# Kernel optimization log

Hardware: AMD Instinct MI355X
Metric: run time of the kernel (lower is better)

## Reference

```python
import jax, jax.numpy as jnp
import numpy as np

BN_EPS = 1e-5


def setup_inputs() -> dict:
    key = jax.random.key(0)
    ks = jax.random.split(key, 6)
    b, c_out, c_high = 8, 256, 512
    h1 = w1 = 64
    h2 = w2 = 32
    return {
        "fms_low": jax.random.normal(ks[0], (b, c_out, h1, w1), jnp.float32),
        "fms_high": jax.random.normal(ks[1], (b, c_high, h2, w2), jnp.float32),
        "w_conv": jax.random.normal(ks[2], (c_out, c_high), jnp.float32) * (1.0 / np.sqrt(c_high)),
        "bn_gamma": jnp.ones((c_out,), jnp.float32),
        "bn_beta": jnp.zeros((c_out,), jnp.float32),
        "bn_mean": jnp.zeros((c_out,), jnp.float32),
        "bn_var": jnp.ones((c_out,), jnp.float32),
        "fc1_w": jax.random.normal(ks[3], (c_out // 4, c_out), jnp.float32) * (1.0 / np.sqrt(c_out)),
        "fc1_b": jnp.zeros((c_out // 4,), jnp.float32),
        "fc2_w": jax.random.normal(ks[4], (c_out // 4, c_out), jnp.float32) * (1.0 / np.sqrt(c_out)),
        "fc2_b": jnp.zeros((c_out // 4,), jnp.float32),
        "scale": jax.random.normal(ks[5], (1,), jnp.float32),
    }


def reference(fms_low, fms_high, w_conv, bn_gamma, bn_beta, bn_mean, bn_var,
              fc1_w, fc1_b, fc2_w, fc2_b, scale):
    b, c, h1, w1 = fms_low.shape
    # conv_high: 1x1 conv (no bias) + BN (inference) + ReLU
    x = jnp.einsum('bchw,oc->bohw', fms_high, w_conv)  # [b, 256, h2, w2]
    inv = bn_gamma / jnp.sqrt(bn_var + BN_EPS)
    x = x * inv[None, :, None, None] + (bn_beta - bn_mean * inv)[None, :, None, None]
    x = jax.nn.relu(x)
    # raw row-major reshapes, matching torch .view(b, -1, C)
    feat_low = fms_low.reshape(b, -1, c)    # [b, N_low, 256]
    feat_high = x.reshape(b, -1, c)         # [b, N_high, 256]
    mid_low = feat_low @ fc1_w.T + fc1_b    # [b, N_low, 64]
    mid_high = feat_high @ fc2_w.T + fc2_b  # [b, N_high, 64]
    energy = jnp.einsum('bnd,bmd->bnm', mid_low, mid_high)  # [b, N_low, N_high]
    attn = jax.nn.softmax(energy, axis=-1)
    # bmm(feat_high^T, attn^T) -> [b, 256, N_low]
    mid = jnp.einsum('bmc,bnm->bcn', feat_high, attn).reshape(b, c, h1, w1)
    return scale[0] * mid
```

## Files before the change

kernel.cpp:

```cpp
#include <hip/hip_runtime.h>
#include <hip/hip_bf16.h>

typedef __bf16 v8bf __attribute__((ext_vector_type(8)));
typedef float  v4f  __attribute__((ext_vector_type(4)));

typedef __attribute__((address_space(3))) void       lds_vd;
typedef __attribute__((address_space(1))) const void gbl_vd;

#define MFMA16(a, b, c) __builtin_amdgcn_mfma_f32_16x16x32_bf16(a, b, c, 0, 0, 0)

__device__ __forceinline__ void split_hl(float v, __bf16* h, __bf16* l) {
    __bf16 hh = (__bf16)v;
    *h = hh;
    *l = (__bf16)(v - (float)hh);
}

__device__ __forceinline__ int swz_idx(int row, int col) {
    return row * 64 + ((((col >> 3) ^ (row & 7))) << 3) + (col & 7);
}
__device__ __forceinline__ const __bf16* frag_ptr(const __bf16* base, int row, int g) {
    return base + row * 64 + ((g ^ (row & 7)) << 3);
}


__global__ __launch_bounds__(256) void k_conv(
    const float* __restrict__ FH, const float* __restrict__ W,
    const float* __restrict__ gamma, const float* __restrict__ beta,
    const float* __restrict__ mean, const float* __restrict__ var,
    __bf16* __restrict__ Xhi, __bf16* __restrict__ Xlo, __bf16* __restrict__ VT)
{
    __shared__ __align__(16) __bf16 Ah[64 * 64];
    __shared__ __align__(16) __bf16 Al[64 * 64];
    __shared__ __align__(16) __bf16 Bh[64 * 64];
    __shared__ __align__(16) __bf16 Bl[64 * 64];
    __shared__ float invl[64], shl[64];

    const int tid = threadIdx.x, lane = tid & 63, w = tid >> 6;
    const int l15 = lane & 15, quad = lane >> 4;
    const int u0 = blockIdx.x * 16, o0 = blockIdx.y * 64, b = blockIdx.z;
    const float* FHb = FH + (size_t)b * 524288;

    if (tid < 64) {
        const int o = o0 + tid;
        const float iv = gamma[o] * rsqrtf(var[o] + 1e-5f);
        invl[tid] = iv;
        shl[tid] = beta[o] - mean[o] * iv;
    }

    const int ao = tid >> 2, aseg = tid & 3;
    float wreg[16], freg[16];
    {
        const float* wp = W + (size_t)(o0 + ao) * 512 + aseg * 16;
        #pragma unroll
        for (int q = 0; q < 4; ++q) {
            float4 f = ((const float4*)wp)[q];
            wreg[4*q] = f.x; wreg[4*q+1] = f.y; wreg[4*q+2] = f.z; wreg[4*q+3] = f.w;
        }
        const float* fp = FHb + (size_t)lane * 1024 + w * 256 + u0;
        #pragma unroll
        for (int q = 0; q < 4; ++q) {
            float4 f = ((const float4*)fp)[q];
            freg[4*q] = f.x; freg[4*q+1] = f.y; freg[4*q+2] = f.z; freg[4*q+3] = f.w;
        }
    }

    v4f acc[2][2];
    #pragma unroll
    for (int i = 0; i < 2; ++i)
        #pragma unroll
        for (int j = 0; j < 2; ++j) { v4f z = {0.f,0.f,0.f,0.f}; acc[i][j] = z; }
    const int oh = w >> 1, nh = w & 1;

    for (int ch = 0; ch < 8; ++ch) {
        if (ch) __syncthreads();
        #pragma unroll
        for (int z = 0; z < 2; ++z) {
            v8bf hv, lv;
            #pragma unroll
            for (int e = 0; e < 8; ++e) {
                __bf16 h, l; split_hl(wreg[8*z + e], &h, &l);
                hv[e] = h; lv[e] = l;
            }
            const int gi = (2*aseg + z) ^ (ao & 7);
            *(v8bf*)(Ah + ao*64 + (gi << 3)) = hv;
            *(v8bf*)(Al + ao*64 + (gi << 3)) = lv;
        }
        #pragma unroll
        for (int ul = 0; ul < 16; ++ul) {
            __bf16 h, l; split_hl(freg[ul], &h, &l);
            const int idx = (w*16 + ul)*64 + (((lane >> 3) ^ (ul & 7)) << 3) + (lane & 7);
            Bh[idx] = h; Bl[idx] = l;
        }
        __syncthreads();
        if (ch < 7) {
            const int c1 = (ch + 1) * 64;
            const float* wp = W + (size_t)(o0 + ao) * 512 + c1 + aseg * 16;
            #pragma unroll
            for (int q = 0; q < 4; ++q) {
                float4 f = ((const float4*)wp)[q];
                wreg[4*q] = f.x; wreg[4*q+1] = f.y; wreg[4*q+2] = f.z; wreg[4*q+3] = f.w;
            }
            const float* fp = FHb + (size_t)(c1 + lane) * 1024 + w * 256 + u0;
            #pragma unroll
            for (int q = 0; q < 4; ++q) {
                float4 f = ((const float4*)fp)[q];
                freg[4*q] = f.x; freg[4*q+1] = f.y; freg[4*q+2] = f.z; freg[4*q+3] = f.w;
            }
        }
        #pragma unroll
        for (int ks = 0; ks < 2; ++ks) {
            const int g = 4*ks + quad;
            v8bf a_h[2], a_l[2], b_h[2], b_l[2];
            #pragma unroll
            for (int i = 0; i < 2; ++i) {
                const int row = oh*32 + i*16 + l15;
                a_h[i] = *(const v8bf*)frag_ptr(Ah, row, g);
                a_l[i] = *(const v8bf*)frag_ptr(Al, row, g);
            }
            #pragma unroll
            for (int j = 0; j < 2; ++j) {
                const int row = nh*32 + j*16 + l15;
                b_h[j] = *(const v8bf*)frag_ptr(Bh, row, g);
                b_l[j] = *(const v8bf*)frag_ptr(Bl, row, g);
            }
            #pragma unroll
            for (int i = 0; i < 2; ++i)
                #pragma unroll
                for (int j = 0; j < 2; ++j) {
                    acc[i][j] = MFMA16(a_h[i], b_h[j], acc[i][j]);
                    acc[i][j] = MFMA16(a_h[i], b_l[j], acc[i][j]);
                    acc[i][j] = MFMA16(a_l[i], b_h[j], acc[i][j]);
                }
        }
    }
    __syncthreads();

    #pragma unroll
    for (int i = 0; i < 2; ++i)
        #pragma unroll
        for (int j = 0; j < 2; ++j)
            #pragma unroll
            for (int r = 0; r < 4; ++r) {
                const int row = oh*32 + i*16 + quad*4 + r;
                const int col = nh*32 + j*16 + l15;
                float v = acc[i][j][r] * invl[row] + shl[row];
                v = fmaxf(v, 0.f);
                __bf16 h, l; split_hl(v, &h, &l);
                const int idx = swz_idx(row, col);
                Ah[idx] = h; Al[idx] = l;
            }
    __syncthreads();
    {
        const int o = tid >> 2, pv = tid & 3;
        const size_t gbase = ((size_t)b*256 + o0 + o) * 1024 + pv*256 + u0;
        #pragma unroll
        for (int z = 0; z < 2; ++z) {
            const int gi = (2*pv + z) ^ (o & 7);
            v8bf h = *(v8bf*)(Ah + o*64 + (gi << 3));
            v8bf l = *(v8bf*)(Al + o*64 + (gi << 3));
            *(v8bf*)(Xhi + gbase + z*8) = h;
            *(v8bf*)(Xlo + gbase + z*8) = l;
        }
    }
    {
        const int ul = tid >> 4, s = tid & 15;
        __bf16 tmp[16];
        #pragma unroll
        for (int k = 0; k < 16; ++k) {
            const int m = s*16 + k;
            const int row = m >> 2;
            const int col = (m & 3)*16 + ul;
            tmp[k] = Ah[swz_idx(row, col)];
        }
        __bf16* vp = VT + ((size_t)b*256 + u0 + ul) * 1024 + 4*o0 + s*16;
        *(v8bf*)(vp)     = *(v8bf*)(tmp);
        *(v8bf*)(vp + 8) = *(v8bf*)(tmp + 8);
    }
}

__global__ __launch_bounds__(256) void k_proj32(
    const float* __restrict__ Feat, const float* __restrict__ Wfc,
    const float* __restrict__ bfc,
    __bf16* __restrict__ Ohi, __bf16* __restrict__ Olo)
{
    __shared__ __align__(16) __bf16 Ah[128 * 64], Al[128 * 64];
    __shared__ __align__(16) __bf16 Bh[64 * 64],  Bl[64 * 64];
    const int tid = threadIdx.x, lane = tid & 63, w = tid >> 6;
    const int l15 = lane & 15, quad = lane >> 4;
    const int r0 = blockIdx.x * 128;
    const int arow = tid >> 1, ahalf = tid & 1;
    const int brow = tid >> 2, bseg = tid & 3;

    float areg[32], breg[16];
    {
        const float* ap = Feat + (size_t)(r0 + arow) * 256 + ahalf * 32;
        #pragma unroll
        for (int q = 0; q < 8; ++q) {
            float4 f = ((const float4*)ap)[q];
            areg[4*q] = f.x; areg[4*q+1] = f.y; areg[4*q+2] = f.z; areg[4*q+3] = f.w;
        }
        const float* bp = Wfc + (size_t)brow * 256 + bseg * 16;
        #pragma unroll
        for (int q = 0; q < 4; ++q) {
            float4 f = ((const float4*)bp)[q];
            breg[4*q] = f.x; breg[4*q+1] = f.y; breg[4*q+2] = f.z; breg[4*q+3] = f.w;
        }
    }
    v4f acc[2][4];
    #pragma unroll
    for (int i = 0; i < 2; ++i)
        #pragma unroll
        for (int j = 0; j < 4; ++j) { v4f z = {0.f,0.f,0.f,0.f}; acc[i][j] = z; }

    for (int ch = 0; ch < 4; ++ch) {
        if (ch) __syncthreads();
        #pragma unroll
        for (int z = 0; z < 4; ++z) {
            v8bf hv, lv;
            #pragma unroll
            for (int e = 0; e < 8; ++e) {
                __bf16 h, l; split_hl(areg[8*z + e], &h, &l);
                hv[e] = h; lv[e] = l;
            }
            const int gi = (4*ahalf + z) ^ (arow & 7);
            *(v8bf*)(Ah + arow*64 + (gi << 3)) = hv;
            *(v8bf*)(Al + arow*64 + (gi << 3)) = lv;
        }
        #pragma unroll
        for (int z = 0; z < 2; ++z) {
            v8bf hv, lv;
            #pragma unroll
            for (int e = 0; e < 8; ++e) {
                __bf16 h, l; split_hl(breg[8*z + e], &h, &l);
                hv[e] = h; lv[e] = l;
            }
            const int gi = (2*bseg + z) ^ (brow & 7);
            *(v8bf*)(Bh + brow*64 + (gi << 3)) = hv;
            *(v8bf*)(Bl + brow*64 + (gi << 3)) = lv;
        }
        __syncthreads();
        if (ch < 3) {
            const int c1 = (ch + 1) * 64;
            const float* ap = Feat + (size_t)(r0 + arow) * 256 + c1 + ahalf * 32;
            #pragma unroll
            for (int q = 0; q < 8; ++q) {
                float4 f = ((const float4*)ap)[q];
                areg[4*q] = f.x; areg[4*q+1] = f.y; areg[4*q+2] = f.z; areg[4*q+3] = f.w;
            }
            const float* bp = Wfc + (size_t)brow * 256 + c1 + bseg * 16;
            #pragma unroll
            for (int q = 0; q < 4; ++q) {
                float4 f = ((const float4*)bp)[q];
                breg[4*q] = f.x; breg[4*q+1] = f.y; breg[4*q+2] = f.z; breg[4*q+3] = f.w;
            }
        }
        #pragma unroll
        for (int ks = 0; ks < 2; ++ks) {
            const int g = 4*ks + quad;
            v8bf a_h[2], a_l[2], b_h[4], b_l[4];
            #pragma unroll
            for (int i = 0; i < 2; ++i) {
                const int row = w*32 + i*16 + l15;
                a_h[i] = *(const v8bf*)frag_ptr(Ah, row, g);
                a_l[i] = *(const v8bf*)frag_ptr(Al, row, g);
            }
            #pragma unroll
            for (int j = 0; j < 4; ++j) {
                const int row = j*16 + l15;
                b_h[j] = *(const v8bf*)frag_ptr(Bh, row, g);
                b_l[j] = *(const v8bf*)frag_ptr(Bl, row, g);
            }
            #pragma unroll
            for (int i = 0; i < 2; ++i)
                #pragma unroll
                for (int j = 0; j < 4; ++j) {
                    acc[i][j] = MFMA16(a_h[i], b_h[j], acc[i][j]);
                    acc[i][j] = MFMA16(a_h[i], b_l[j], acc[i][j]);
                    acc[i][j] = MFMA16(a_l[i], b_h[j], acc[i][j]);
                }
        }
    }
    __syncthreads();
    #pragma unroll
    for (int j = 0; j < 4; ++j) {
        const float bias = bfc[j*16 + l15];
        #pragma unroll
        for (int i = 0; i < 2; ++i)
            #pragma unroll
            for (int r = 0; r < 4; ++r) {
                const int row = w*32 + i*16 + quad*4 + r;
                const int col = j*16 + l15;
                __bf16 h, l; split_hl(acc[i][j][r] + bias, &h, &l);
                const int idx = swz_idx(row, col);
                Ah[idx] = h; Al[idx] = l;
            }
    }
    __syncthreads();
    {
        const int row = tid >> 1, half = tid & 1;
        __bf16* oh_ = Ohi + (size_t)(r0 + row) * 64 + half * 32;
        __bf16* ol_ = Olo + (size_t)(r0 + row) * 64 + half * 32;
        #pragma unroll
        for (int z = 0; z < 4; ++z) {
            const int gi = (4*half + z) ^ (row & 7);
            *(v8bf*)(oh_ + z*8) = *(v8bf*)(Ah + row*64 + (gi << 3));
            *(v8bf*)(ol_ + z*8) = *(v8bf*)(Al + row*64 + (gi << 3));
        }
    }
}

__global__ __launch_bounds__(256) void k_projbf(
    const __bf16* __restrict__ Fhi, const __bf16* __restrict__ Flo,
    const float* __restrict__ Wfc, const float* __restrict__ bfc,
    __bf16* __restrict__ Ohi, __bf16* __restrict__ Olo)
{
    __shared__ __align__(16) __bf16 Ah[32 * 64], Al[32 * 64];
    __shared__ __align__(16) __bf16 Bh[64 * 64], Bl[64 * 64];
    const int tid = threadIdx.x, lane = tid & 63, w = tid >> 6;
    const int l15 = lane & 15, quad = lane >> 4;
    const int r0 = blockIdx.x * 32;
    const int srow = tid >> 3, sg = tid & 7;
    const int brow = tid >> 2, bseg = tid & 3;

    float breg[16];
    v8bf ha, la;
    {
        ha = *(const v8bf*)(Fhi + (size_t)(r0 + srow) * 256 + sg * 8);
        la = *(const v8bf*)(Flo + (size_t)(r0 + srow) * 256 + sg * 8);
        const float* bp = Wfc + (size_t)brow * 256 + bseg * 16;
        #pragma unroll
        for (int q = 0; q < 4; ++q) {
            float4 f = ((const float4*)bp)[q];
            breg[4*q] = f.x; breg[4*q+1] = f.y; breg[4*q+2] = f.z; breg[4*q+3] = f.w;
        }
    }
    v4f acc[2];
    { v4f z = {0.f,0.f,0.f,0.f}; acc[0] = z; acc[1] = z; }
    const int mt = w >> 1, nh = w & 1;

    for (int ch = 0; ch < 4; ++ch) {
        if (ch) __syncthreads();
        {
            const int gi = sg ^ (srow & 7);
            *(v8bf*)(Ah + srow*64 + (gi << 3)) = ha;
            *(v8bf*)(Al + srow*64 + (gi << 3)) = la;
        }
        #pragma unroll
        for (int z = 0; z < 2; ++z) {
            v8bf hv, lv;
            #pragma unroll
            for (int e = 0; e < 8; ++e) {
                __bf16 h, l; split_hl(breg[8*z + e], &h, &l);
                hv[e] = h; lv[e] = l;
            }
            const int gi = (2*bseg + z) ^ (brow & 7);
            *(v8bf*)(Bh + brow*64 + (gi << 3)) = hv;
            *(v8bf*)(Bl + brow*64 + (gi << 3)) = lv;
        }
        __syncthreads();
        if (ch < 3) {
            const int c1 = (ch + 1) * 64;
            ha = *(const v8bf*)(Fhi + (size_t)(r0 + srow) * 256 + c1 + sg * 8);
            la = *(const v8bf*)(Flo + (size_t)(r0 + srow) * 256 + c1 + sg * 8);
            const float* bp = Wfc + (size_t)brow * 256 + c1 + bseg * 16;
            #pragma unroll
            for (int q = 0; q < 4; ++q) {
                float4 f = ((const float4*)bp)[q];
                breg[4*q] = f.x; breg[4*q+1] = f.y; breg[4*q+2] = f.z; breg[4*q+3] = f.w;
            }
        }
        #pragma unroll
        for (int ks = 0; ks < 2; ++ks) {
            const int g = 4*ks + quad;
            const int arow = mt*16 + l15;
            v8bf a_h = *(const v8bf*)frag_ptr(Ah, arow, g);
            v8bf a_l = *(const v8bf*)frag_ptr(Al, arow, g);
            #pragma unroll
            for (int j = 0; j < 2; ++j) {
                const int row = (nh*2 + j)*16 + l15;
                v8bf b_h = *(const v8bf*)frag_ptr(Bh, row, g);
                v8bf b_l = *(const v8bf*)frag_ptr(Bl, row, g);
                acc[j] = MFMA16(a_h, b_h, acc[j]);
                acc[j] = MFMA16(a_h, b_l, acc[j]);
                acc[j] = MFMA16(a_l, b_h, acc[j]);
            }
        }
    }
    __syncthreads();
    #pragma unroll
    for (int j = 0; j < 2; ++j) {
        const float bias = bfc[(nh*2 + j)*16 + l15];
        #pragma unroll
        for (int r = 0; r < 4; ++r) {
            const int row = mt*16 + quad*4 + r;
            const int col = (nh*2 + j)*16 + l15;
            __bf16 h, l; split_hl(acc[j][r] + bias, &h, &l);
            const int idx = swz_idx(row, col);
            Ah[idx] = h; Al[idx] = l;
        }
    }
    __syncthreads();
    {
        const int row = tid >> 3, g = tid & 7;
        const int gi = g ^ (row & 7);
        *(v8bf*)(Ohi + (size_t)(r0 + row) * 64 + g*8) = *(v8bf*)(Ah + row*64 + (gi << 3));
        *(v8bf*)(Olo + (size_t)(r0 + row) * 64 + g*8) = *(v8bf*)(Al + row*64 + (gi << 3));
    }
}

__global__ __launch_bounds__(512, 4) void k_attn(
    const __bf16* __restrict__ MLhi, const __bf16* __restrict__ MLlo,
    const __bf16* __restrict__ MHhi, const __bf16* __restrict__ MHlo,
    const __bf16* __restrict__ VT,
    const float* __restrict__ scale_p,
    float* __restrict__ out)
{
    __shared__ __align__(16) __bf16 Khi[2][32 * 64];
    __shared__ __align__(16) __bf16 Klo[2][32 * 64];
    __shared__ __align__(16) __bf16 Vs [2][256 * 32];
    __shared__ __align__(16) __bf16 Ps [2][4][16 * 32];
    __shared__ float lsh[2][4][16];

    const int tid = threadIdx.x, lane = tid & 63, w = tid >> 6;
    const int l15 = lane & 15, quad = lane >> 4;
    const int b = blockIdx.x & 7, qtb = blockIdx.x >> 3;
    const int q0 = qtb * 64;
    const int qt = w & 3, mb = w >> 2;

    v8bf qhi[2], qlo[2];
    {
        const __bf16* qp  = MLhi + ((size_t)(b*4096 + q0 + qt*16 + l15)) * 64;
        const __bf16* qlp = MLlo + ((size_t)(b*4096 + q0 + qt*16 + l15)) * 64;
        #pragma unroll
        for (int h = 0; h < 2; ++h) {
            qhi[h] = *(const v8bf*)(qp + h*32 + quad*8);
            qlo[h] = *(const v8bf*)(qlp + h*32 + quad*8);
        }
    }
    #pragma unroll
    for (int h = 0; h < 2; ++h) {
        asm volatile("" : "+v"(qhi[h]));
        asm volatile("" : "+v"(qlo[h]));
    }

    const char* Khg = (const char*)(MHhi + (size_t)b * 65536);
    const char* Klg = (const char*)(MHlo + (size_t)b * 65536);
    const char* Vg  = (const char*)(VT + (size_t)b * 262144);
    const int offK = (lane >> 3) * 128 + (((lane & 7) ^ ((lane >> 3) & 7)) << 4);
    const int offV = (lane >> 2) * 2048 + ((((lane & 3) ^ ((lane >> 3) & 3))) << 4);

    const char* kgsrc = (w < 4) ? Khg : Klg;
    const int ksub = (w & 3) * 1024;

    v4f oacc[4][2];
    #pragma unroll
    for (int t = 0; t < 4; ++t)
        #pragma unroll
        for (int cb = 0; cb < 2; ++cb) { v4f z = {0.f,0.f,0.f,0.f}; oacc[t][cb] = z; }
    float lrow[4] = {0.f, 0.f, 0.f, 0.f};

    {
        char* kdst = (char*)((w < 4) ? &Khi[0][0] : &Klo[0][0]);
        __builtin_amdgcn_global_load_lds((gbl_vd*)(kgsrc + ksub + offK),
                                         (lds_vd*)(kdst + ksub), 16, 0, 0);
        #pragma unroll
        for (int j = 0; j < 2; ++j) {
            const int i = w*2 + j;
            __builtin_amdgcn_global_load_lds((gbl_vd*)(Vg + i*32768 + offV),
                                             (lds_vd*)((char*)&Vs[0][0] + i*1024), 16, 0, 0);
        }
    }
    asm volatile("s_waitcnt vmcnt(2)\n\ts_barrier" ::: "memory");

    for (int ch = 0; ch < 32; ++ch) {
        const int cur = ch & 1, nxt = cur ^ 1;
        const int mn = ((ch < 31) ? (ch + 1) : 31) * 32;

        {
            char* kdst = (char*)((w < 4) ? &Khi[nxt][0] : &Klo[nxt][0]);
            __builtin_amdgcn_global_load_lds((gbl_vd*)(kgsrc + mn*128 + ksub + offK),
                                             (lds_vd*)(kdst + ksub), 16, 0, 0);
        }

        v4f sacc = {0.f, 0.f, 0.f, 0.f};
        __builtin_amdgcn_s_setprio(1);
        #pragma unroll
        for (int h = 0; h < 2; ++h) {
            const int row = mb*16 + l15, g = 4*h + quad;
            v8bf kh = *(const v8bf*)frag_ptr(&Khi[cur][0], row, g);
            v8bf kl = *(const v8bf*)frag_ptr(&Klo[cur][0], row, g);
            sacc = MFMA16(qhi[h], kh, sacc);
            sacc = MFMA16(qhi[h], kl, sacc);
            sacc = MFMA16(qlo[h], kh, sacc);
        }
        __builtin_amdgcn_s_setprio(0);

        #pragma unroll
        for (int r = 0; r < 4; ++r) {
            const float p = __expf(sacc[r]);
            lrow[r] += p;
            const int row = quad*4 + r;
            const int slot = (mb*2 + (l15 >> 3)) ^ ((row >> 1) & 3);
            Ps[cur][qt][row*32 + (slot << 3) + (l15 & 7)] = (__bf16)p;
        }

        if (ch) {
            const int pb = nxt;
            v8bf pa[4];
            #pragma unroll
            for (int t = 0; t < 4; ++t)
                pa[t] = *(const v8bf*)(&Ps[pb][t][0] + l15*32 + ((quad ^ ((l15 >> 1) & 3)) << 3));
            __builtin_amdgcn_s_setprio(1);
            #pragma unroll
            for (int cb = 0; cb < 2; ++cb) {
                const int vrow = w*32 + cb*16 + l15;
                v8bf vv = *(const v8bf*)(&Vs[pb][0] + vrow*32 + ((quad ^ ((vrow >> 1) & 3)) << 3));
                #pragma unroll
                for (int t = 0; t < 4; ++t)
                    oacc[t][cb] = MFMA16(pa[t], vv, oacc[t][cb]);
            }
            __builtin_amdgcn_s_setprio(0);
        }

        asm volatile("s_waitcnt lgkmcnt(0)" ::: "memory");
        #pragma unroll
        for (int j = 0; j < 2; ++j) {
            const int i = w*2 + j;
            __builtin_amdgcn_global_load_lds((gbl_vd*)(Vg + mn*2 + i*32768 + offV),
                                             (lds_vd*)((char*)&Vs[nxt][0] + i*1024), 16, 0, 0);
        }

        asm volatile("s_waitcnt vmcnt(2) lgkmcnt(0)\n\ts_barrier" ::: "memory");
    }

    {
        v8bf pa[4];
        #pragma unroll
        for (int t = 0; t < 4; ++t)
            pa[t] = *(const v8bf*)(&Ps[1][t][0] + l15*32 + ((quad ^ ((l15 >> 1) & 3)) << 3));
        #pragma unroll
        for (int cb = 0; cb < 2; ++cb) {
            const int vrow = w*32 + cb*16 + l15;
            v8bf vv = *(const v8bf*)(&Vs[1][0] + vrow*32 + ((quad ^ ((vrow >> 1) & 3)) << 3));
            #pragma unroll
            for (int t = 0; t < 4; ++t)
                oacc[t][cb] = MFMA16(pa[t], vv, oacc[t][cb]);
        }
    }

    #pragma unroll
    for (int r = 0; r < 4; ++r) {
        float s = lrow[r];
        #pragma unroll
        for (int d = 1; d < 16; d <<= 1) s += __shfl_xor(s, d, 64);
        lrow[r] = s;
    }
    if (l15 == 0) {
        #pragma unroll
        for (int r = 0; r < 4; ++r) lsh[mb][qt][quad*4 + r] = lrow[r];
    }
    __syncthreads();

    const float scl = scale_p[0];
    float inv[4][4];
    #pragma unroll
    for (int t = 0; t < 4; ++t)
        #pragma unroll
        for (int r = 0; r < 4; ++r)
            inv[t][r] = scl / (lsh[0][t][quad*4 + r] + lsh[1][t][quad*4 + r]);
    float* outb = out + (size_t)b * 256 * 4096;
    #pragma unroll
    for (int cb = 0; cb < 2; ++cb) {
        const int c = w*32 + cb*16 + l15;
        #pragma unroll
        for (int t = 0; t < 4; ++t) {
            float4 v;
            v.x = oacc[t][cb][0] * inv[t][0];
            v.y = oacc[t][cb][1] * inv[t][1];
            v.z = oacc[t][cb][2] * inv[t][2];
            v.w = oacc[t][cb][3] * inv[t][3];
            *(float4*)(outb + (size_t)c * 4096 + q0 + t*16 + quad*4) = v;
        }
    }
}

extern "C" void kernel_launch(void* const* d_in, const int* in_sizes, int n_in,
                              void* d_out, int out_size, void* d_ws, size_t ws_size,
                              hipStream_t stream)
{
    const float* fms_low  = (const float*)d_in[0];
    const float* fms_high = (const float*)d_in[1];
    const float* w_conv   = (const float*)d_in[2];
    const float* gamma    = (const float*)d_in[3];
    const float* beta     = (const float*)d_in[4];
    const float* mean     = (const float*)d_in[5];
    const float* var      = (const float*)d_in[6];
    const float* fc1_w    = (const float*)d_in[7];
    const float* fc1_b    = (const float*)d_in[8];
    const float* fc2_w    = (const float*)d_in[9];
    const float* fc2_b    = (const float*)d_in[10];
    const float* scale    = (const float*)d_in[11];
    float* out = (float*)d_out;

    __bf16* Xhi  = (__bf16*)d_ws;
    __bf16* Xlo  = Xhi  + (size_t)8*256*1024;
    __bf16* VT   = Xlo  + (size_t)8*256*1024;
    __bf16* MLhi = VT   + (size_t)8*256*1024;
    __bf16* MLlo = MLhi + (size_t)8*4096*64;
    __bf16* MHhi = MLlo + (size_t)8*4096*64;
    __bf16* MHlo = MHhi + (size_t)8*1024*64;

    k_conv<<<dim3(16, 4, 8), 256, 0, stream>>>(fms_high, w_conv, gamma, beta,
                                               mean, var, Xhi, Xlo, VT);
    k_projbf<<<dim3(256), 256, 0, stream>>>(Xhi, Xlo, fc2_w, fc2_b, MHhi, MHlo);
    k_proj32<<<dim3(256), 256, 0, stream>>>(fms_low, fc1_w, fc1_b, MLhi, MLlo);
    k_attn<<<dim3(512), 512, 0, stream>>>(MLhi, MLlo, MHhi, MHlo, VT, scale, out);
}
```

Measured before the change: 184.0 us.

## Restructure projection kernels to load full weight once and stream activations from registers

Both projection kernels now split the entire 64x256 weight into bf16 hi/lo in LDS once, with a single barrier, instead of re-staging weight and activation chunks in a 4-step loop with two barriers per step. Each wave takes 16 rows and loads its A fragments straight from global into registers, prefetching the next k-chunk. The epilogue goes through a small per-wave LDS buffer without block-wide syncs. Row tiles change to 64 rows per block, giving 512 blocks for the low path and 128 for the high path. This cuts barriers and LDS staging of activations, but each block now fills a larger weight tile and uses more LDS, which may lower occupancy.

```diff
diff --git a/kernel.cpp b/kernel.cpp
--- a/kernel.cpp
+++ b/kernel.cpp
@@ -183,129 +183,107 @@
     const float* __restrict__ bfc,
     __bf16* __restrict__ Ohi, __bf16* __restrict__ Olo)
 {
-    __shared__ __align__(16) __bf16 Ah[128 * 64], Al[128 * 64];
-    __shared__ __align__(16) __bf16 Bh[64 * 64],  Bl[64 * 64];
+    __shared__ __align__(16) __bf16 Bh[64 * 256];
+    __shared__ __align__(16) __bf16 Bl[64 * 256];
+    __shared__ __align__(16) __bf16 Eo[4][16 * 64];
+
     const int tid = threadIdx.x, lane = tid & 63, w = tid >> 6;
     const int l15 = lane & 15, quad = lane >> 4;
-    const int r0 = blockIdx.x * 128;
-    const int arow = tid >> 1, ahalf = tid & 1;
-    const int brow = tid >> 2, bseg = tid & 3;
-
-    float areg[32], breg[16];
-    {
-        const float* ap = Feat + (size_t)(r0 + arow) * 256 + ahalf * 32;
-        #pragma unroll
-        for (int q = 0; q < 8; ++q) {
-            float4 f = ((const float4*)ap)[q];
-            areg[4*q] = f.x; areg[4*q+1] = f.y; areg[4*q+2] = f.z; areg[4*q+3] = f.w;
-        }
-        const float* bp = Wfc + (size_t)brow * 256 + bseg * 16;
-        #pragma unroll
-        for (int q = 0; q < 4; ++q) {
-            float4 f = ((const float4*)bp)[q];
-            breg[4*q] = f.x; breg[4*q+1] = f.y; breg[4*q+2] = f.z; breg[4*q+3] = f.w;
-        }
-    }
-    v4f acc[2][4];
-    #pragma unroll
-    for (int i = 0; i < 2; ++i)
-        #pragma unroll
-        for (int j = 0; j < 4; ++j) { v4f z = {0.f,0.f,0.f,0.f}; acc[i][j] = z; }
-
-    for (int ch = 0; ch < 4; ++ch) {
-        if (ch) __syncthreads();
-        #pragma unroll
-        for (int z = 0; z < 4; ++z) {
+    const int r0 = blockIdx.x * 64;
+    const int row = r0 + w*16 + l15;
+
+    const float* ap = Feat + (size_t)row * 256 + quad * 8;
+    float acur[8], anxt[8];
+    {
+        float4 f0 = ((const float4*)ap)[0];
+        float4 f1 = ((const float4*)ap)[1];
+        acur[0]=f0.x; acur[1]=f0.y; acur[2]=f0.z; acur[3]=f0.w;
+        acur[4]=f1.x; acur[5]=f1.y; acur[6]=f1.z; acur[7]=f1.w;
+    }
+
+    {
+        const int n = tid >> 2, q4 = tid & 3, n7 = n & 7;
+        const float* wp = Wfc + (size_t)n * 256 + q4 * 64;
+        #pragma unroll
+        for (int z = 0; z < 8; ++z) {
+            float4 f0 = ((const float4*)wp)[2*z];
+            float4 f1 = ((const float4*)wp)[2*z + 1];
+            float w8[8] = {f0.x, f0.y, f0.z, f0.w, f1.x, f1.y, f1.z, f1.w};
             v8bf hv, lv;
             #pragma unroll
             for (int e = 0; e < 8; ++e) {
-                __bf16 h, l; split_hl(areg[8*z + e], &h, &l);
+                __bf16 h, l; split_hl(w8[e], &h, &l);
                 hv[e] = h; lv[e] = l;
             }
-            const int gi = (4*ahalf + z) ^ (arow & 7);
-            *(v8bf*)(Ah + arow*64 + (gi << 3)) = hv;
-            *(v8bf*)(Al + arow*64 + (gi << 3)) = lv;
-        }
-        #pragma unroll
-        for (int z = 0; z < 2; ++z) {
-            v8bf hv, lv;
-            #pragma unroll
-            for (int e = 0; e < 8; ++e) {
-                __bf16 h, l; split_hl(breg[8*z + e], &h, &l);
-                hv[e] = h; lv[e] = l;
-            }
-            const int gi = (2*bseg + z) ^ (brow & 7);
-            *(v8bf*)(Bh + brow*64 + (gi << 3)) = hv;
-            *(v8bf*)(Bl + brow*64 + (gi << 3)) = lv;
-        }
-        __syncthreads();
-        if (ch < 3) {
-            const int c1 = (ch + 1) * 64;
-            const float* ap = Feat + (size_t)(r0 + arow) * 256 + c1 + ahalf * 32;
-            #pragma unroll
-            for (int q = 0; q < 8; ++q) {
-                float4 f = ((const float4*)ap)[q];
-                areg[4*q] = f.x; areg[4*q+1] = f.y; areg[4*q+2] = f.z; areg[4*q+3] = f.w;
-            }
-            const float* bp = Wfc + (size_t)brow * 256 + c1 + bseg * 16;
-            #pragma unroll
-            for (int q = 0; q < 4; ++q) {
-                float4 f = ((const float4*)bp)[q];
-                breg[4*q] = f.x; breg[4*q+1] = f.y; breg[4*q+2] = f.z; breg[4*q+3] = f.w;
-            }
-        }
-        #pragma unroll
-        for (int ks = 0; ks < 2; ++ks) {
-            const int g = 4*ks + quad;
-            v8bf a_h[2], a_l[2], b_h[4], b_l[4];
-            #pragma unroll
-            for (int i = 0; i < 2; ++i) {
-                const int row = w*32 + i*16 + l15;
-                a_h[i] = *(const v8bf*)frag_ptr(Ah, row, g);
-                a_l[i] = *(const v8bf*)frag_ptr(Al, row, g);
-            }
-            #pragma unroll
-            for (int j = 0; j < 4; ++j) {
-                const int row = j*16 + l15;
-                b_h[j] = *(const v8bf*)frag_ptr(Bh, row, g);
-                b_l[j] = *(const v8bf*)frag_ptr(Bl, row, g);
-            }
-            #pragma unroll
-            for (int i = 0; i < 2; ++i)
-                #pragma unroll
-                for (int j = 0; j < 4; ++j) {
-                    acc[i][j] = MFMA16(a_h[i], b_h[j], acc[i][j]);
-                    acc[i][j] = MFMA16(a_h[i], b_l[j], acc[i][j]);
-                    acc[i][j] = MFMA16(a_l[i], b_h[j], acc[i][j]);
-                }
+            const int gsw = (q4*8 + z) ^ n7;
+            *(v8bf*)(Bh + n*256 + gsw*8) = hv;
+            *(v8bf*)(Bl + n*256 + gsw*8) = lv;
         }
     }
     __syncthreads();
+
+    v4f acc[4];
+    #pragma unroll
+    for (int j = 0; j < 4; ++j) { v4f z = {0.f,0.f,0.f,0.f}; acc[j] = z; }
+
+    const int l7 = l15 & 7;
+    const __bf16* bh_base = Bh + l15*256;
+    const __bf16* bl_base = Bl + l15*256;
+
+    #pragma unroll
+    for (int kc = 0; kc < 8; ++kc) {
+        if (kc < 7) {
+            float4 f0 = ((const float4*)(ap + (kc+1)*32))[0];
+            float4 f1 = ((const float4*)(ap + (kc+1)*32))[1];
+            anxt[0]=f0.x; anxt[1]=f0.y; anxt[2]=f0.z; anxt[3]=f0.w;
+            anxt[4]=f1.x; anxt[5]=f1.y; anxt[6]=f1.z; anxt[7]=f1.w;
+        }
+        v8bf ah, al;
+        #pragma unroll
+        for (int e = 0; e < 8; ++e) {
+            __bf16 h, l; split_hl(acur[e], &h, &l);
+            ah[e] = h; al[e] = l;
+        }
+        const int goff = (((kc*4 + quad) ^ l7) << 3);
+        #pragma unroll
+        for (int j = 0; j < 4; ++j) {
+            v8bf bh = *(const v8bf*)(bh_base + j*4096 + goff);
+            v8bf bl = *(const v8bf*)(bl_base + j*4096 + goff);
+            acc[j] = MFMA16(ah, bh, acc[j]);
+            acc[j] = MFMA16(ah, bl, acc[j]);
+            acc[j] = MFMA16(al, bh, acc[j]);
+        }
+        #pragma unroll
+        for (int e = 0; e < 8; ++e) acur[e] = anxt[e];
+    }
+
+    __bf16* eo = &Eo[w][0];
+    __bf16 lb[4][4];
     #pragma unroll
     for (int j = 0; j < 4; ++j) {
         const float bias = bfc[j*16 + l15];
         #pragma unroll
-        for (int i = 0; i < 2; ++i)
-            #pragma unroll
-            for (int r = 0; r < 4; ++r) {
-                const int row = w*32 + i*16 + quad*4 + r;
-                const int col = j*16 + l15;
-                __bf16 h, l; split_hl(acc[i][j][r] + bias, &h, &l);
-                const int idx = swz_idx(row, col);
-                Ah[idx] = h; Al[idx] = l;
-            }
-    }
-    __syncthreads();
-    {
-        const int row = tid >> 1, half = tid & 1;
-        __bf16* oh_ = Ohi + (size_t)(r0 + row) * 64 + half * 32;
-        __bf16* ol_ = Olo + (size_t)(r0 + row) * 64 + half * 32;
-        #pragma unroll
-        for (int z = 0; z < 4; ++z) {
-            const int gi = (4*half + z) ^ (row & 7);
-            *(v8bf*)(oh_ + z*8) = *(v8bf*)(Ah + row*64 + (gi << 3));
-            *(v8bf*)(ol_ + z*8) = *(v8bf*)(Al + row*64 + (gi << 3));
-        }
+        for (int r = 0; r < 4; ++r) {
+            __bf16 h, l; split_hl(acc[j][r] + bias, &h, &l);
+            lb[j][r] = l;
+            eo[swz_idx(quad*4 + r, j*16 + l15)] = h;
+        }
+    }
+    const size_t orow = (size_t)row * 64;
+    #pragma unroll
+    for (int z = 0; z < 2; ++z) {
+        const int gi = (2*quad + z) ^ l7;
+        *(v8bf*)(Ohi + orow + quad*16 + z*8) = *(v8bf*)(eo + l15*64 + gi*8);
+    }
+    #pragma unroll
+    for (int j = 0; j < 4; ++j)
+        #pragma unroll
+        for (int r = 0; r < 4; ++r)
+            eo[swz_idx(quad*4 + r, j*16 + l15)] = lb[j][r];
+    #pragma unroll
+    for (int z = 0; z < 2; ++z) {
+        const int gi = (2*quad + z) ^ l7;
+        *(v8bf*)(Olo + orow + quad*16 + z*8) = *(v8bf*)(eo + l15*64 + gi*8);
     }
 }
 
@@ -314,97 +292,95 @@
     const float* __restrict__ Wfc, const float* __restrict__ bfc,
     __bf16* __restrict__ Ohi, __bf16* __restrict__ Olo)
 {
-    __shared__ __align__(16) __bf16 Ah[32 * 64], Al[32 * 64];
-    __shared__ __align__(16) __bf16 Bh[64 * 64], Bl[64 * 64];
+    __shared__ __align__(16) __bf16 Bh[64 * 256];
+    __shared__ __align__(16) __bf16 Bl[64 * 256];
+    __shared__ __align__(16) __bf16 Eo[4][16 * 64];
+
     const int tid = threadIdx.x, lane = tid & 63, w = tid >> 6;
     const int l15 = lane & 15, quad = lane >> 4;
-    const int r0 = blockIdx.x * 32;
-    const int srow = tid >> 3, sg = tid & 7;
-    const int brow = tid >> 2, bseg = tid & 3;
-
-    float breg[16];
-    v8bf ha, la;
-    {
-        ha = *(const v8bf*)(Fhi + (size_t)(r0 + srow) * 256 + sg * 8);
-        la = *(const v8bf*)(Flo + (size_t)(r0 + srow) * 256 + sg * 8);
-        const float* bp = Wfc + (size_t)brow * 256 + bseg * 16;
-        #pragma unroll
-        for (int q = 0; q < 4; ++q) {
-            float4 f = ((const float4*)bp)[q];
-            breg[4*q] = f.x; breg[4*q+1] = f.y; breg[4*q+2] = f.z; breg[4*q+3] = f.w;
-        }
-    }
-    v4f acc[2];
-    { v4f z = {0.f,0.f,0.f,0.f}; acc[0] = z; acc[1] = z; }
-    const int mt = w >> 1, nh = w & 1;
-
-    for (int ch = 0; ch < 4; ++ch) {
-        if (ch) __syncthreads();
-        {
-            const int gi = sg ^ (srow & 7);
-            *(v8bf*)(Ah + srow*64 + (gi << 3)) = ha;
-            *(v8bf*)(Al + srow*64 + (gi << 3)) = la;
-        }
-        #pragma unroll
-        for (int z = 0; z < 2; ++z) {
+    const int r0 = blockIdx.x * 64;
+    const int row = r0 + w*16 + l15;
+
+    const __bf16* fh = Fhi + (size_t)row * 256 + quad * 8;
+    const __bf16* fl = Flo + (size_t)row * 256 + quad * 8;
+    v8bf ah = *(const v8bf*)(fh);
+    v8bf al = *(const v8bf*)(fl);
+
+    {
+        const int n = tid >> 2, q4 = tid & 3, n7 = n & 7;
+        const float* wp = Wfc + (size_t)n * 256 + q4 * 64;
+        #pragma unroll
+        for (int z = 0; z < 8; ++z) {
+            float4 f0 = ((const float4*)wp)[2*z];
+            float4 f1 = ((const float4*)wp)[2*z + 1];
+            float w8[8] = {f0.x, f0.y, f0.z, f0.w, f1.x, f1.y, f1.z, f1.w};
             v8bf hv, lv;
             #pragma unroll
             for (int e = 0; e < 8; ++e) {
-                __bf16 h, l; split_hl(breg[8*z + e], &h, &l);
+                __bf16 h, l; split_hl(w8[e], &h, &l);
                 hv[e] = h; lv[e] = l;
             }
-            const int gi = (2*bseg + z) ^ (brow & 7);
-            *(v8bf*)(Bh + brow*64 + (gi << 3)) = hv;
-            *(v8bf*)(Bl + brow*64 + (gi << 3)) = lv;
-        }
-        __syncthreads();
-        if (ch < 3) {
-            const int c1 = (ch + 1) * 64;
-            ha = *(const v8bf*)(Fhi + (size_t)(r0 + srow) * 256 + c1 + sg * 8);
-            la = *(const v8bf*)(Flo + (size_t)(r0 + srow) * 256 + c1 + sg * 8);
-            const float* bp = Wfc + (size_t)brow * 256 + c1 + bseg * 16;
-            #pragma unroll
-            for (int q = 0; q < 4; ++q) {
-                float4 f = ((const float4*)bp)[q];
-                breg[4*q] = f.x; breg[4*q+1] = f.y; breg[4*q+2] = f.z; breg[4*q+3] = f.w;
-            }
-        }
-        #pragma unroll
-        for (int ks = 0; ks < 2; ++ks) {
-            const int g = 4*ks + quad;
-            const int arow = mt*16 + l15;
-            v8bf a_h = *(const v8bf*)frag_ptr(Ah, arow, g);
-            v8bf a_l = *(const v8bf*)frag_ptr(Al, arow, g);
-            #pragma unroll
-            for (int j = 0; j < 2; ++j) {
-                const int row = (nh*2 + j)*16 + l15;
-                v8bf b_h = *(const v8bf*)frag_ptr(Bh, row, g);
-                v8bf b_l = *(const v8bf*)frag_ptr(Bl, row, g);
-                acc[j] = MFMA16(a_h, b_h, acc[j]);
-                acc[j] = MFMA16(a_h, b_l, acc[j]);
-                acc[j] = MFMA16(a_l, b_h, acc[j]);
-            }
+            const int gsw = (q4*8 + z) ^ n7;
+            *(v8bf*)(Bh + n*256 + gsw*8) = hv;
+            *(v8bf*)(Bl + n*256 + gsw*8) = lv;
         }
     }
     __syncthreads();
-    #pragma unroll
-    for (int j = 0; j < 2; ++j) {
-        const float bias = bfc[(nh*2 + j)*16 + l15];
+
+    v4f acc[4];
+    #pragma unroll
+    for (int j = 0; j < 4; ++j) { v4f z = {0.f,0.f,0.f,0.f}; acc[j] = z; }
+
+    const int l7 = l15 & 7;
+    const __bf16* bh_base = Bh + l15*256;
+    const __bf16* bl_base = Bl + l15*256;
+
+    #pragma unroll
+    for (int kc = 0; kc < 8; ++kc) {
+        v8bf anh, anl;
+        if (kc < 7) {
+            anh = *(const v8bf*)(fh + (kc+1)*32);
+            anl = *(const v8bf*)(fl + (kc+1)*32);
+        }
+        const int goff = (((kc*4 + quad) ^ l7) << 3);
+        #pragma unroll
+        for (int j = 0; j < 4; ++j) {
+            v8bf bh = *(const v8bf*)(bh_base + j*4096 + goff);
+            v8bf bl = *(const v8bf*)(bl_base + j*4096 + goff);
+            acc[j] = MFMA16(ah, bh, acc[j]);
+            acc[j] = MFMA16(ah, bl, acc[j]);
+            acc[j] = MFMA16(al, bh, acc[j]);
+        }
+        if (kc < 7) { ah = anh; al = anl; }
+    }
+
+    __bf16* eo = &Eo[w][0];
+    __bf16 lb[4][4];
+    #pragma unroll
+    for (int j = 0; j < 4; ++j) {
+        const float bias = bfc[j*16 + l15];
         #pragma unroll
         for (int r = 0; r < 4; ++r) {
-            const int row = mt*16 + quad*4 + r;
-            const int col = (nh*2 + j)*16 + l15;
             __bf16 h, l; split_hl(acc[j][r] + bias, &h, &l);
-            const int idx = swz_idx(row, col);
-            Ah[idx] = h; Al[idx] = l;
-        }
-    }
-    __syncthreads();
-    {
-        const int row = tid >> 3, g = tid & 7;
-        const int gi = g ^ (row & 7);
-        *(v8bf*)(Ohi + (size_t)(r0 + row) * 64 + g*8) = *(v8bf*)(Ah + row*64 + (gi << 3));
-        *(v8bf*)(Olo + (size_t)(r0 + row) * 64 + g*8) = *(v8bf*)(Al + row*64 + (gi << 3));
+            lb[j][r] = l;
+            eo[swz_idx(quad*4 + r, j*16 + l15)] = h;
+        }
+    }
+    const size_t orow = (size_t)row * 64;
+    #pragma unroll
+    for (int z = 0; z < 2; ++z) {
+        const int gi = (2*quad + z) ^ l7;
+        *(v8bf*)(Ohi + orow + quad*16 + z*8) = *(v8bf*)(eo + l15*64 + gi*8);
+    }
+    #pragma unroll
+    for (int j = 0; j < 4; ++j)
+        #pragma unroll
+        for (int r = 0; r < 4; ++r)
+            eo[swz_idx(quad*4 + r, j*16 + l15)] = lb[j][r];
+    #pragma unroll
+    for (int z = 0; z < 2; ++z) {
+        const int gi = (2*quad + z) ^ l7;
+        *(v8bf*)(Olo + orow + quad*16 + z*8) = *(v8bf*)(eo + l15*64 + gi*8);
     }
 }
 
@@ -612,7 +588,7 @@
 
     k_conv<<<dim3(16, 4, 8), 256, 0, stream>>>(fms_high, w_conv, gamma, beta,
                                                mean, var, Xhi, Xlo, VT);
-    k_projbf<<<dim3(256), 256, 0, stream>>>(Xhi, Xlo, fc2_w, fc2_b, MHhi, MHlo);
-    k_proj32<<<dim3(256), 256, 0, stream>>>(fms_low, fc1_w, fc1_b, MLhi, MLlo);
+    k_projbf<<<dim3(128), 256, 0, stream>>>(Xhi, Xlo, fc2_w, fc2_b, MHhi, MHlo);
+    k_proj32<<<dim3(512), 256, 0, stream>>>(fms_low, fc1_w, fc1_b, MLhi, MLlo);
     k_attn<<<dim3(512), 512, 0, stream>>>(MLhi, MLlo, MHhi, MHlo, VT, scale, out);
 }
```

Measured after the change: 184.8 us. Within noise of the previous version (+0.5%).
